# Kernel tuning notes

Measured on AMD Instinct MI355X. Metric: run time of the kernel, lower is better.

Reference implementation:

```python
import jax, jax.numpy as jnp
import numpy as np

N_NODES = 50000
N_EDGES = 800000
D_FEAT = 64
N_CLASSES = 40


def setup_inputs() -> dict:
    key = jax.random.key(0)
    ks = jax.random.split(key, 8)
    x = jax.random.normal(ks[0], (N_NODES, D_FEAT), dtype=jnp.float32)
    edge_index = jax.random.randint(ks[1], (2, N_EDGES), 0, N_NODES, dtype=jnp.int64)
    # GCNConv weights (glorot-ish scale) and post-aggregation biases
    s1 = 1.0 / np.sqrt(D_FEAT)
    W1 = jax.random.normal(ks[2], (D_FEAT, D_FEAT), dtype=jnp.float32) * s1
    b1 = jnp.zeros((D_FEAT,), dtype=jnp.float32)
    W2 = jax.random.normal(ks[3], (D_FEAT, D_FEAT), dtype=jnp.float32) * s1
    b2 = jnp.zeros((D_FEAT,), dtype=jnp.float32)
    W3 = jax.random.normal(ks[4], (D_FEAT, N_CLASSES), dtype=jnp.float32) * s1
    b3 = jnp.zeros((N_CLASSES,), dtype=jnp.float32)
    return {"x": x, "edge_index": edge_index, "W1": W1, "b1": b1,
            "W2": W2, "b2": b2, "W3": W3, "b3": b3}


def _gcn_layer(x, src, dst, norm, W, b, n_nodes):
    # dense transform then normalized neighbor aggregation (PyG GCNConv)
    h = x @ W                                   # [N, out]
    msgs = h[src] * norm[:, None]               # gather over edges [E+N, out]
    agg = jax.ops.segment_sum(msgs, dst, num_segments=n_nodes)
    return agg + b


def reference(x, edge_index, W1, b1, W2, b2, W3, b3):
    n = x.shape[0]
    loops = jnp.arange(n, dtype=edge_index.dtype)
    src = jnp.concatenate([edge_index[0], loops])   # add self-loops
    dst = jnp.concatenate([edge_index[1], loops])
    # symmetric normalization: deg over targets incl. self-loops
    deg = jax.ops.segment_sum(jnp.ones_like(dst, dtype=x.dtype), dst, num_segments=n)
    dinv = jnp.where(deg > 0, jax.lax.rsqrt(deg), 0.0)
    norm = dinv[src] * dinv[dst]                    # [E+N]
    for W, b in ((W1, b1), (W2, b2), (W3, b3)):
        x = jax.nn.relu(_gcn_layer(x, src, dst, norm, W, b, n))
        # dropout treated as identity (deterministic eval reference)
    return jax.nn.log_softmax(x, axis=-1)
```

## Files before the change

kernel.cpp:

```cpp
#include <hip/hip_runtime.h>
#include <math.h>


#define DF 64
#define TB 256
#define NPART 8

__device__ __forceinline__ unsigned short f2bf(float f) {
    union { float f; unsigned u; } c; c.f = f;
    unsigned u = c.u;
    return (unsigned short)((u + 0x7fffu + ((u >> 16) & 1u)) >> 16);
}
__device__ __forceinline__ float bf2f(unsigned short h) {
    union { unsigned u; float f; } c; c.u = ((unsigned)h) << 16;
    return c.f;
}
__device__ __forceinline__ void acc_bf16x4(uint2 v, float* a) {
    a[0] += bf2f((unsigned short)(v.x & 0xffffu));
    a[1] += bf2f((unsigned short)(v.x >> 16));
    a[2] += bf2f((unsigned short)(v.y & 0xffffu));
    a[3] += bf2f((unsigned short)(v.y >> 16));
}

__global__ void zero_int_kernel(int* __restrict__ p, int n) {
    int i = blockIdx.x * blockDim.x + threadIdx.x;
    if (i < n) p[i] = 0;
}

__global__ void count_deg_part_kernel(const int* __restrict__ dst, int* __restrict__ deg,
                                      int e, int psize) {
    const int p   = blockIdx.x & (NPART - 1);
    const int sl  = blockIdx.x / NPART;
    const int nsl = gridDim.x / NPART;
    const int lo = p * psize, hi = lo + psize;
    for (int i = sl * TB + threadIdx.x; i < e; i += nsl * TB) {
        int d = dst[i];
        if (d >= lo && d < hi) atomicAdd(&deg[d], 1);
    }
}

__global__ void scan_block_kernel(const int* __restrict__ deg, int* __restrict__ ex,
                                  int* __restrict__ bsum, float* __restrict__ dinv, int n) {
    __shared__ int s[TB];
    const int t = threadIdx.x;
    const int i = blockIdx.x * TB + t;
    int v = (i < n) ? deg[i] : 0;
    if (i < n) dinv[i] = rsqrtf((float)(v + 1));
    s[t] = v; __syncthreads();
#pragma unroll
    for (int o = 1; o < TB; o <<= 1) {
        int u = (t >= o) ? s[t - o] : 0;
        __syncthreads();
        s[t] += u;
        __syncthreads();
    }
    if (i < n) ex[i] = s[t] - v;
    if (t == TB - 1) bsum[blockIdx.x] = s[TB - 1];
}

__global__ void add_offsets_kernel(int* __restrict__ ex, const int* __restrict__ bsum,
                                   int* __restrict__ cursor, int n, int nb) {
    __shared__ int s[TB];
    const int t = threadIdx.x;
    int v = (t < nb) ? bsum[t] : 0;
    s[t] = v; __syncthreads();
#pragma unroll
    for (int o = 1; o < TB; o <<= 1) {
        int u = (t >= o) ? s[t - o] : 0;
        __syncthreads();
        s[t] += u;
        __syncthreads();
    }
    const int boff = (blockIdx.x > 0) ? s[blockIdx.x - 1] : 0;
    const int i = blockIdx.x * TB + t;
    if (i < n) {
        int r = ex[i] + boff;
        ex[i] = r;
        cursor[i] = r;
    }
}

__global__ void fill_csr_part_kernel(const int* __restrict__ src, const int* __restrict__ dst,
                                     int* __restrict__ cursor,
                                     unsigned short* __restrict__ cidx, int e, int psize) {
    const int p   = blockIdx.x & (NPART - 1);
    const int sl  = blockIdx.x / NPART;
    const int nsl = gridDim.x / NPART;
    const int lo = p * psize, hi = lo + psize;
    for (int i = sl * TB + threadIdx.x; i < e; i += nsl * TB) {
        int d = dst[i];
        if (d >= lo && d < hi) {
            int pos = atomicAdd(&cursor[d], 1);
            cidx[pos] = (unsigned short)src[i];
        }
    }
}

template <int NC, typename TIN>
__global__ __launch_bounds__(256) void gemm_kernel(const TIN* __restrict__ X,
                                                   const float* __restrict__ W,
                                                   const float* __restrict__ dinv,
                                                   unsigned short* __restrict__ G, int M) {
    __shared__ float Ws[64 * NC];
    __shared__ float Xs[16][65];
    const int tx = threadIdx.x;
    const int ty = threadIdx.y;
    const int tid = ty * 16 + tx;
    for (int i = tid; i < 64 * NC / 4; i += 256)
        ((float4*)Ws)[i] = ((const float4*)W)[i];
    const int row0 = blockIdx.x * 16;
    {
        int r = tid / 16, c4 = tid % 16;
        bool ok = (row0 + r < M);
        if (sizeof(TIN) == 4) {
            const float* Xf = (const float*)X;
            float4 v = ok ? ((const float4*)(Xf + (size_t)(row0 + r) * 64))[c4]
                          : make_float4(0.f, 0.f, 0.f, 0.f);
            Xs[r][c4 * 4 + 0] = v.x; Xs[r][c4 * 4 + 1] = v.y;
            Xs[r][c4 * 4 + 2] = v.z; Xs[r][c4 * 4 + 3] = v.w;
        } else {
            const unsigned short* Xh = (const unsigned short*)X;
            ushort4 v = ok ? ((const ushort4*)(Xh + (size_t)(row0 + r) * 64))[c4]
                           : make_ushort4(0, 0, 0, 0);
            Xs[r][c4 * 4 + 0] = bf2f(v.x); Xs[r][c4 * 4 + 1] = bf2f(v.y);
            Xs[r][c4 * 4 + 2] = bf2f(v.z); Xs[r][c4 * 4 + 3] = bf2f(v.w);
        }
    }
    __syncthreads();
    const int row = row0 + ty;
    const int c0 = tx * 4;
    if (row < M && c0 < NC) {
        float a0 = 0.f, a1 = 0.f, a2 = 0.f, a3 = 0.f;
#pragma unroll
        for (int k = 0; k < 64; ++k) {
            float xk = Xs[ty][k];
            float4 w = ((const float4*)(Ws + (size_t)k * NC))[tx];
            a0 += xk * w.x; a1 += xk * w.y; a2 += xk * w.z; a3 += xk * w.w;
        }
        float di = dinv[row];
        ushort4 o;
        o.x = f2bf(a0 * di); o.y = f2bf(a1 * di);
        o.z = f2bf(a2 * di); o.w = f2bf(a3 * di);
        *((ushort4*)(G + (size_t)row * NC + c0)) = o;
    }
}

template <int NC, typename TOUT, bool LSM>
__global__ void agg_kernel(const unsigned short* __restrict__ G,
                           const int* __restrict__ rowptr, const int* __restrict__ deg,
                           const unsigned short* __restrict__ cidx,
                           const float* __restrict__ dinv, const float* __restrict__ b,
                           TOUT* __restrict__ Y, int M) {
    constexpr int NQ = NC / 4;
    const int lane = threadIdx.x & 63;
    const int node = blockIdx.x * 4 + (threadIdx.x >> 6);
    if (node >= M) return;
    const int grp = lane >> 4;
    const int sub = lane & 15;
    const bool act = (sub < NQ);
    const int start = rowptr[node];
    const int cnt = deg[node];

    float a[4] = {0.f, 0.f, 0.f, 0.f};
    float c[4] = {0.f, 0.f, 0.f, 0.f};

    for (int base = 0; base < cnt; base += 64) {
        const int nthis = min(64, cnt - base);
        int myidx = (lane < nthis) ? (int)cidx[start + base + lane] : 0;
        int j = 0;
        for (; j + 8 <= nthis; j += 8) {
            int s0 = __shfl(myidx, j + grp, 64);
            int s1 = __shfl(myidx, j + 4 + grp, 64);
            if (act) {
                uint2 v0 = *(const uint2*)(G + (size_t)s0 * NC + sub * 4);
                uint2 v1 = *(const uint2*)(G + (size_t)s1 * NC + sub * 4);
                acc_bf16x4(v0, a);
                acc_bf16x4(v1, c);
            }
        }
        if (j + 4 <= nthis) {
            int s0 = __shfl(myidx, j + grp, 64);
            if (act) {
                uint2 v0 = *(const uint2*)(G + (size_t)s0 * NC + sub * 4);
                acc_bf16x4(v0, a);
            }
            j += 4;
        }
        const int rem = nthis - j;
        if (grp < rem) {
            int s0 = __shfl(myidx, j + grp, 64);
            if (act) {
                uint2 v0 = *(const uint2*)(G + (size_t)s0 * NC + sub * 4);
                acc_bf16x4(v0, c);
            }
        }
    }
#pragma unroll
    for (int k = 0; k < 4; ++k) a[k] += c[k];
#pragma unroll
    for (int k = 0; k < 4; ++k) {
        a[k] += __shfl_xor(a[k], 16, 64);
        a[k] += __shfl_xor(a[k], 32, 64);
    }
    float v[4];
    {
        float self[4] = {0.f, 0.f, 0.f, 0.f};
        float4 bb = make_float4(0.f, 0.f, 0.f, 0.f);
        if (act) {
            uint2 sv = *(const uint2*)(G + (size_t)node * NC + sub * 4);
            self[0] = bf2f((unsigned short)(sv.x & 0xffffu));
            self[1] = bf2f((unsigned short)(sv.x >> 16));
            self[2] = bf2f((unsigned short)(sv.y & 0xffffu));
            self[3] = bf2f((unsigned short)(sv.y >> 16));
            bb = *(const float4*)(b + sub * 4);
        }
        const float di = dinv[node];
        v[0] = fmaxf((a[0] + self[0]) * di + bb.x, 0.f);
        v[1] = fmaxf((a[1] + self[1]) * di + bb.y, 0.f);
        v[2] = fmaxf((a[2] + self[2]) * di + bb.z, 0.f);
        v[3] = fmaxf((a[3] + self[3]) * di + bb.w, 0.f);
    }

    if (!LSM) {
        if (act && grp == 0) {
            if (sizeof(TOUT) == 2) {
                ushort4 o;
                o.x = f2bf(v[0]); o.y = f2bf(v[1]); o.z = f2bf(v[2]); o.w = f2bf(v[3]);
                *((ushort4*)((unsigned short*)Y + (size_t)node * NC + sub * 4)) = o;
            } else {
                *((float4*)((float*)Y + (size_t)node * NC + sub * 4)) =
                    make_float4(v[0], v[1], v[2], v[3]);
            }
        }
        return;
    }
    float m = act ? fmaxf(fmaxf(v[0], v[1]), fmaxf(v[2], v[3])) : -INFINITY;
#pragma unroll
    for (int o = 1; o < 16; o <<= 1) m = fmaxf(m, __shfl_xor(m, o, 64));
    float es = act ? (expf(v[0] - m) + expf(v[1] - m) + expf(v[2] - m) + expf(v[3] - m)) : 0.f;
#pragma unroll
    for (int o = 1; o < 16; o <<= 1) es += __shfl_xor(es, o, 64);
    const float ls = logf(es);
    if (act && grp == 0) {
        *((float4*)((float*)Y + (size_t)node * NC + sub * 4)) =
            make_float4(v[0] - m - ls, v[1] - m - ls, v[2] - m - ls, v[3] - m - ls);
    }
}

extern "C" void kernel_launch(void* const* d_in, const int* in_sizes, int n_in,
                              void* d_out, int out_size, void* d_ws, size_t ws_size,
                              hipStream_t stream) {
    const float* x  = (const float*)d_in[0];
    const int*   ei = (const int*)d_in[1];
    const float* W1 = (const float*)d_in[2];
    const float* b1 = (const float*)d_in[3];
    const float* W2 = (const float*)d_in[4];
    const float* b2 = (const float*)d_in[5];
    const float* W3 = (const float*)d_in[6];
    const float* b3 = (const float*)d_in[7];
    float* out = (float*)d_out;

    const int M  = in_sizes[0] / DF;
    const int E  = in_sizes[1] / 2;
    (void)ws_size; (void)n_in; (void)out_size;

    const int* src = ei;
    const int* dst = ei + E;

    const size_t Ma = ((size_t)M + 63) & ~63ull;
    const size_t Ea = ((size_t)E + 63) & ~63ull;

    int* deg    = (int*)d_ws;
    int* rowptr = deg + Ma;
    int* cursor = rowptr + Ma;
    int* bsum   = cursor + Ma;
    unsigned short* cidx = (unsigned short*)(bsum + 256);
    float* dinv = (float*)(cidx + Ea);
    unsigned short* G    = (unsigned short*)(dinv + Ma);
    unsigned short* Bact = G + Ma * DF;

    const int gN = (M + TB - 1) / TB;
    const int nb = gN;
    const int psize = (M + NPART - 1) / NPART;
    const int partGrd = NPART * 96;

    zero_int_kernel<<<gN, TB, 0, stream>>>(deg, M);
    count_deg_part_kernel<<<partGrd, TB, 0, stream>>>(dst, deg, E, psize);
    scan_block_kernel<<<nb, TB, 0, stream>>>(deg, rowptr, bsum, dinv, M);
    add_offsets_kernel<<<nb, TB, 0, stream>>>(rowptr, bsum, cursor, M, nb);
    fill_csr_part_kernel<<<partGrd, TB, 0, stream>>>(src, dst, cursor, cidx, E, psize);

    const dim3 gemmBlk(16, 16);
    const int  gemmGrd = (M + 15) / 16;
    const int  aggGrd  = (M + 3) / 4;

    gemm_kernel<64, float><<<gemmGrd, gemmBlk, 0, stream>>>(x, W1, dinv, G, M);
    agg_kernel<64, unsigned short, false><<<aggGrd, TB, 0, stream>>>(G, rowptr, deg, cidx, dinv, b1, Bact, M);
    gemm_kernel<64, unsigned short><<<gemmGrd, gemmBlk, 0, stream>>>(Bact, W2, dinv, G, M);
    agg_kernel<64, unsigned short, false><<<aggGrd, TB, 0, stream>>>(G, rowptr, deg, cidx, dinv, b2, Bact, M);
    gemm_kernel<40, unsigned short><<<gemmGrd, gemmBlk, 0, stream>>>(Bact, W3, dinv, G, M);
    agg_kernel<40, float, true><<<aggGrd, TB, 0, stream>>>(G, rowptr, deg, cidx, dinv, b3, out, M);
}
```

Measured before the change: 214.9 us.

## Register-tile GEMM to 4x4 per thread and widen 64-col aggregation to 16-byte loads

The dense transform kernel now handles 64 rows per block, with each thread computing a 4x4 output tile. This reuses each loaded weight vector across four rows and loads bf16 inputs 16 bytes at a time. The 64-feature aggregation gets its own kernel in which each lane gathers 8 bf16 values with uint4 loads, so 8 neighbors are covered per wave step instead of 4. The trade-off is more registers for the accumulators and 4x fewer GEMM blocks, which could reduce occupancy.

```diff
diff --git a/kernel.cpp b/kernel.cpp
--- a/kernel.cpp
+++ b/kernel.cpp
@@ -14,6 +14,19 @@
 __device__ __forceinline__ float bf2f(unsigned short h) {
     union { unsigned u; float f; } c; c.u = ((unsigned)h) << 16;
     return c.f;
+}
+__device__ __forceinline__ unsigned pk2bf(float lo, float hi) {
+    return (unsigned)f2bf(lo) | ((unsigned)f2bf(hi) << 16);
+}
+__device__ __forceinline__ void acc_bf16x8(uint4 v, float* a) {
+    a[0] += bf2f((unsigned short)(v.x & 0xffffu));
+    a[1] += bf2f((unsigned short)(v.x >> 16));
+    a[2] += bf2f((unsigned short)(v.y & 0xffffu));
+    a[3] += bf2f((unsigned short)(v.y >> 16));
+    a[4] += bf2f((unsigned short)(v.z & 0xffffu));
+    a[5] += bf2f((unsigned short)(v.z >> 16));
+    a[6] += bf2f((unsigned short)(v.w & 0xffffu));
+    a[7] += bf2f((unsigned short)(v.w >> 16));
 }
 __device__ __forceinline__ void acc_bf16x4(uint2 v, float* a) {
     a[0] += bf2f((unsigned short)(v.x & 0xffffu));
@@ -102,56 +115,154 @@
                                                    const float* __restrict__ dinv,
                                                    unsigned short* __restrict__ G, int M) {
     __shared__ float Ws[64 * NC];
-    __shared__ float Xs[16][65];
+    __shared__ float Xs[64][65];
     const int tx = threadIdx.x;
     const int ty = threadIdx.y;
     const int tid = ty * 16 + tx;
-    for (int i = tid; i < 64 * NC / 4; i += 256)
+    for (int i = tid; i < 16 * NC; i += 256)
         ((float4*)Ws)[i] = ((const float4*)W)[i];
-    const int row0 = blockIdx.x * 16;
-    {
-        int r = tid / 16, c4 = tid % 16;
-        bool ok = (row0 + r < M);
-        if (sizeof(TIN) == 4) {
-            const float* Xf = (const float*)X;
-            float4 v = ok ? ((const float4*)(Xf + (size_t)(row0 + r) * 64))[c4]
-                          : make_float4(0.f, 0.f, 0.f, 0.f);
-            Xs[r][c4 * 4 + 0] = v.x; Xs[r][c4 * 4 + 1] = v.y;
-            Xs[r][c4 * 4 + 2] = v.z; Xs[r][c4 * 4 + 3] = v.w;
-        } else {
-            const unsigned short* Xh = (const unsigned short*)X;
-            ushort4 v = ok ? ((const ushort4*)(Xh + (size_t)(row0 + r) * 64))[c4]
-                           : make_ushort4(0, 0, 0, 0);
-            Xs[r][c4 * 4 + 0] = bf2f(v.x); Xs[r][c4 * 4 + 1] = bf2f(v.y);
-            Xs[r][c4 * 4 + 2] = bf2f(v.z); Xs[r][c4 * 4 + 3] = bf2f(v.w);
+    const int row0 = blockIdx.x * 64;
+    if (sizeof(TIN) == 4) {
+        const float* Xf = (const float*)X;
+#pragma unroll
+        for (int i = tid; i < 1024; i += 256) {
+            int r = i >> 4, q = i & 15;
+            float4 v = (row0 + r < M) ? ((const float4*)(Xf + (size_t)(row0 + r) * 64))[q]
+                                      : make_float4(0.f, 0.f, 0.f, 0.f);
+            Xs[r][q * 4 + 0] = v.x; Xs[r][q * 4 + 1] = v.y;
+            Xs[r][q * 4 + 2] = v.z; Xs[r][q * 4 + 3] = v.w;
+        }
+    } else {
+        const unsigned short* Xh = (const unsigned short*)X;
+#pragma unroll
+        for (int i = tid; i < 512; i += 256) {
+            int r = i >> 3, s = i & 7;
+            uint4 v = (row0 + r < M)
+                        ? *(const uint4*)(Xh + (size_t)(row0 + r) * 64 + s * 8)
+                        : make_uint4(0, 0, 0, 0);
+            Xs[r][s * 8 + 0] = bf2f((unsigned short)(v.x & 0xffffu));
+            Xs[r][s * 8 + 1] = bf2f((unsigned short)(v.x >> 16));
+            Xs[r][s * 8 + 2] = bf2f((unsigned short)(v.y & 0xffffu));
+            Xs[r][s * 8 + 3] = bf2f((unsigned short)(v.y >> 16));
+            Xs[r][s * 8 + 4] = bf2f((unsigned short)(v.z & 0xffffu));
+            Xs[r][s * 8 + 5] = bf2f((unsigned short)(v.z >> 16));
+            Xs[r][s * 8 + 6] = bf2f((unsigned short)(v.w & 0xffffu));
+            Xs[r][s * 8 + 7] = bf2f((unsigned short)(v.w >> 16));
         }
     }
     __syncthreads();
-    const int row = row0 + ty;
-    const int c0 = tx * 4;
-    if (row < M && c0 < NC) {
-        float a0 = 0.f, a1 = 0.f, a2 = 0.f, a3 = 0.f;
-#pragma unroll
-        for (int k = 0; k < 64; ++k) {
-            float xk = Xs[ty][k];
-            float4 w = ((const float4*)(Ws + (size_t)k * NC))[tx];
-            a0 += xk * w.x; a1 += xk * w.y; a2 += xk * w.z; a3 += xk * w.w;
-        }
-        float di = dinv[row];
-        ushort4 o;
-        o.x = f2bf(a0 * di); o.y = f2bf(a1 * di);
-        o.z = f2bf(a2 * di); o.w = f2bf(a3 * di);
-        *((ushort4*)(G + (size_t)row * NC + c0)) = o;
-    }
-}
-
-template <int NC, typename TOUT, bool LSM>
-__global__ void agg_kernel(const unsigned short* __restrict__ G,
-                           const int* __restrict__ rowptr, const int* __restrict__ deg,
-                           const unsigned short* __restrict__ cidx,
-                           const float* __restrict__ dinv, const float* __restrict__ b,
-                           TOUT* __restrict__ Y, int M) {
-    constexpr int NQ = NC / 4;
+    if (tx * 4 >= NC) return;
+    float acc[4][4];
+#pragma unroll
+    for (int i = 0; i < 4; ++i)
+#pragma unroll
+        for (int j = 0; j < 4; ++j) acc[i][j] = 0.f;
+#pragma unroll
+    for (int k = 0; k < 64; ++k) {
+        float4 w = ((const float4*)(Ws + (size_t)k * NC))[tx];
+        float x0 = Xs[ty * 4 + 0][k];
+        float x1 = Xs[ty * 4 + 1][k];
+        float x2 = Xs[ty * 4 + 2][k];
+        float x3 = Xs[ty * 4 + 3][k];
+        acc[0][0] += x0 * w.x; acc[0][1] += x0 * w.y; acc[0][2] += x0 * w.z; acc[0][3] += x0 * w.w;
+        acc[1][0] += x1 * w.x; acc[1][1] += x1 * w.y; acc[1][2] += x1 * w.z; acc[1][3] += x1 * w.w;
+        acc[2][0] += x2 * w.x; acc[2][1] += x2 * w.y; acc[2][2] += x2 * w.z; acc[2][3] += x2 * w.w;
+        acc[3][0] += x3 * w.x; acc[3][1] += x3 * w.y; acc[3][2] += x3 * w.z; acc[3][3] += x3 * w.w;
+    }
+#pragma unroll
+    for (int i = 0; i < 4; ++i) {
+        const int row = row0 + ty * 4 + i;
+        if (row < M) {
+            const float di = dinv[row];
+            ushort4 o;
+            o.x = f2bf(acc[i][0] * di); o.y = f2bf(acc[i][1] * di);
+            o.z = f2bf(acc[i][2] * di); o.w = f2bf(acc[i][3] * di);
+            *((ushort4*)(G + (size_t)row * NC + tx * 4)) = o;
+        }
+    }
+}
+
+__global__ void agg64_kernel(const unsigned short* __restrict__ G,
+                             const int* __restrict__ rowptr, const int* __restrict__ deg,
+                             const unsigned short* __restrict__ cidx,
+                             const float* __restrict__ dinv, const float* __restrict__ b,
+                             unsigned short* __restrict__ Y, int M) {
+    const int lane = threadIdx.x & 63;
+    const int node = blockIdx.x * 4 + (threadIdx.x >> 6);
+    if (node >= M) return;
+    const int grp = lane >> 3;
+    const int sub = lane & 7;
+    const int start = rowptr[node];
+    const int cnt = deg[node];
+
+    float a[8] = {0.f, 0.f, 0.f, 0.f, 0.f, 0.f, 0.f, 0.f};
+    float c[8] = {0.f, 0.f, 0.f, 0.f, 0.f, 0.f, 0.f, 0.f};
+
+    for (int base = 0; base < cnt; base += 64) {
+        const int nthis = min(64, cnt - base);
+        int myidx = (lane < nthis) ? (int)cidx[start + base + lane] : 0;
+        int j = 0;
+        for (; j + 16 <= nthis; j += 16) {
+            int s0 = __shfl(myidx, j + grp, 64);
+            int s1 = __shfl(myidx, j + 8 + grp, 64);
+            uint4 v0 = *(const uint4*)(G + (size_t)s0 * 64 + sub * 8);
+            uint4 v1 = *(const uint4*)(G + (size_t)s1 * 64 + sub * 8);
+            acc_bf16x8(v0, a);
+            acc_bf16x8(v1, c);
+        }
+        if (j + 8 <= nthis) {
+            int s0 = __shfl(myidx, j + grp, 64);
+            uint4 v0 = *(const uint4*)(G + (size_t)s0 * 64 + sub * 8);
+            acc_bf16x8(v0, a);
+            j += 8;
+        }
+        const int rem = nthis - j;
+        if (grp < rem) {
+            int s0 = __shfl(myidx, j + grp, 64);
+            uint4 v0 = *(const uint4*)(G + (size_t)s0 * 64 + sub * 8);
+            acc_bf16x8(v0, c);
+        }
+    }
+#pragma unroll
+    for (int k = 0; k < 8; ++k) a[k] += c[k];
+#pragma unroll
+    for (int k = 0; k < 8; ++k) {
+        a[k] += __shfl_xor(a[k], 8, 64);
+        a[k] += __shfl_xor(a[k], 16, 64);
+        a[k] += __shfl_xor(a[k], 32, 64);
+    }
+    if (grp != 0) return;
+    uint4 sv = *(const uint4*)(G + (size_t)node * 64 + sub * 8);
+    float self[8];
+    self[0] = bf2f((unsigned short)(sv.x & 0xffffu)); self[1] = bf2f((unsigned short)(sv.x >> 16));
+    self[2] = bf2f((unsigned short)(sv.y & 0xffffu)); self[3] = bf2f((unsigned short)(sv.y >> 16));
+    self[4] = bf2f((unsigned short)(sv.z & 0xffffu)); self[5] = bf2f((unsigned short)(sv.z >> 16));
+    self[6] = bf2f((unsigned short)(sv.w & 0xffffu)); self[7] = bf2f((unsigned short)(sv.w >> 16));
+    float4 b0 = *(const float4*)(b + sub * 8);
+    float4 b1 = *(const float4*)(b + sub * 8 + 4);
+    const float di = dinv[node];
+    float v[8];
+    v[0] = fmaxf((a[0] + self[0]) * di + b0.x, 0.f);
+    v[1] = fmaxf((a[1] + self[1]) * di + b0.y, 0.f);
+    v[2] = fmaxf((a[2] + self[2]) * di + b0.z, 0.f);
+    v[3] = fmaxf((a[3] + self[3]) * di + b0.w, 0.f);
+    v[4] = fmaxf((a[4] + self[4]) * di + b1.x, 0.f);
+    v[5] = fmaxf((a[5] + self[5]) * di + b1.y, 0.f);
+    v[6] = fmaxf((a[6] + self[6]) * di + b1.z, 0.f);
+    v[7] = fmaxf((a[7] + self[7]) * di + b1.w, 0.f);
+    uint4 o;
+    o.x = pk2bf(v[0], v[1]); o.y = pk2bf(v[2], v[3]);
+    o.z = pk2bf(v[4], v[5]); o.w = pk2bf(v[6], v[7]);
+    *((uint4*)(Y + (size_t)node * 64 + sub * 8)) = o;
+}
+
+__global__ void agg40_lsm_kernel(const unsigned short* __restrict__ G,
+                                 const int* __restrict__ rowptr, const int* __restrict__ deg,
+                                 const unsigned short* __restrict__ cidx,
+                                 const float* __restrict__ dinv, const float* __restrict__ b,
+                                 float* __restrict__ Y, int M) {
+    constexpr int NC = 40;
+    constexpr int NQ = 10;
     const int lane = threadIdx.x & 63;
     const int node = blockIdx.x * 4 + (threadIdx.x >> 6);
     if (node >= M) return;
@@ -220,20 +331,6 @@
         v[2] = fmaxf((a[2] + self[2]) * di + bb.z, 0.f);
         v[3] = fmaxf((a[3] + self[3]) * di + bb.w, 0.f);
     }
-
-    if (!LSM) {
-        if (act && grp == 0) {
-            if (sizeof(TOUT) == 2) {
-                ushort4 o;
-                o.x = f2bf(v[0]); o.y = f2bf(v[1]); o.z = f2bf(v[2]); o.w = f2bf(v[3]);
-                *((ushort4*)((unsigned short*)Y + (size_t)node * NC + sub * 4)) = o;
-            } else {
-                *((float4*)((float*)Y + (size_t)node * NC + sub * 4)) =
-                    make_float4(v[0], v[1], v[2], v[3]);
-            }
-        }
-        return;
-    }
     float m = act ? fmaxf(fmaxf(v[0], v[1]), fmaxf(v[2], v[3])) : -INFINITY;
 #pragma unroll
     for (int o = 1; o < 16; o <<= 1) m = fmaxf(m, __shfl_xor(m, o, 64));
@@ -242,7 +339,7 @@
     for (int o = 1; o < 16; o <<= 1) es += __shfl_xor(es, o, 64);
     const float ls = logf(es);
     if (act && grp == 0) {
-        *((float4*)((float*)Y + (size_t)node * NC + sub * 4)) =
+        *((float4*)(Y + (size_t)node * NC + sub * 4)) =
             make_float4(v[0] - m - ls, v[1] - m - ls, v[2] - m - ls, v[3] - m - ls);
     }
 }
@@ -291,13 +388,13 @@
     fill_csr_part_kernel<<<partGrd, TB, 0, stream>>>(src, dst, cursor, cidx, E, psize);
 
     const dim3 gemmBlk(16, 16);
-    const int  gemmGrd = (M + 15) / 16;
+    const int  gemmGrd = (M + 63) / 64;
     const int  aggGrd  = (M + 3) / 4;
 
     gemm_kernel<64, float><<<gemmGrd, gemmBlk, 0, stream>>>(x, W1, dinv, G, M);
-    agg_kernel<64, unsigned short, false><<<aggGrd, TB, 0, stream>>>(G, rowptr, deg, cidx, dinv, b1, Bact, M);
+    agg64_kernel<<<aggGrd, TB, 0, stream>>>(G, rowptr, deg, cidx, dinv, b1, Bact, M);
     gemm_kernel<64, unsigned short><<<gemmGrd, gemmBlk, 0, stream>>>(Bact, W2, dinv, G, M);
-    agg_kernel<64, unsigned short, false><<<aggGrd, TB, 0, stream>>>(G, rowptr, deg, cidx, dinv, b2, Bact, M);
+    agg64_kernel<<<aggGrd, TB, 0, stream>>>(G, rowptr, deg, cidx, dinv, b2, Bact, M);
     gemm_kernel<40, unsigned short><<<gemmGrd, gemmBlk, 0, stream>>>(Bact, W3, dinv, G, M);
-    agg_kernel<40, float, true><<<aggGrd, TB, 0, stream>>>(G, rowptr, deg, cidx, dinv, b3, out, M);
-}
+    agg40_lsm_kernel<<<aggGrd, TB, 0, stream>>>(G, rowptr, deg, cidx, dinv, b3, out, M);
+}
```

Result: slower. 249.8 us (+16.2%).
